# Performance work log

Hardware: AMD Instinct MI355X
Metric: run time of the kernel (lower is better)

The kernel has to match this reference:

```python
import jax, jax.numpy as jnp
import numpy as np

N = 30000; F = 16; E = 300000
HD = 256; NH = 8; C = HD // NH; L = 3
S = 256; K = 128
NH_CA = 4; HDC = HD // NH_CA


def _ln(x, g, b):
    mu = jnp.mean(x, -1, keepdims=True)
    v = jnp.mean((x - mu) ** 2, -1, keepdims=True)
    return (x - mu) / jnp.sqrt(v + 1e-5) * g + b


def setup_inputs() -> dict:
    ks = iter(jax.random.split(jax.random.key(0), 64))
    def nrm(sh, s=0.05):
        return jax.random.normal(next(ks), sh, jnp.float32) * s
    def zeros(sh):
        return jnp.zeros(sh, jnp.float32)
    def ones(sh):
        return jnp.ones(sh, jnp.float32)
    inp = {}
    inp['x'] = jax.random.normal(next(ks), (N, F), jnp.float32)
    inp['edge_index'] = jax.random.randint(next(ks), (2, E), 0, N, jnp.int32)
    inp['batch'] = jnp.zeros((N,), jnp.int32)
    inp['sheet_node_idx'] = jax.random.randint(next(ks), (S, K), 0, N, jnp.int32)
    inp['sheet_features'] = jax.random.normal(next(ks), (S, F), jnp.float32)
    # pre_transform
    inp['pre_W'] = nrm((F, HD)); inp['pre_b'] = zeros((HD,))
    # stacked GATv2 layers (lin_l, lin_r, att, bias)
    inp['gat_Wl'] = nrm((L, HD, HD)); inp['gat_Wr'] = nrm((L, HD, HD))
    inp['gat_att'] = nrm((L, NH, C)); inp['gat_b'] = zeros((L, HD))
    # geometry encoder
    inp['geo_W1'] = nrm((F, HD)); inp['geo_b1'] = zeros((HD,))
    inp['geo_g1'] = ones((HD,)); inp['geo_be1'] = zeros((HD,))
    inp['geo_W2'] = nrm((HD, HD)); inp['geo_b2'] = zeros((HD,))
    inp['geo_g2'] = ones((HD,)); inp['geo_be2'] = zeros((HD,))
    # cross attention (4 heads)
    inp['ca_Wq'] = nrm((HD, HD)); inp['ca_bq'] = zeros((HD,))
    inp['ca_Wk'] = nrm((HD, HD)); inp['ca_bk'] = zeros((HD,))
    inp['ca_Wv'] = nrm((HD, HD)); inp['ca_bv'] = zeros((HD,))
    inp['ca_Wo'] = nrm((HD, HD)); inp['ca_bo'] = zeros((HD,))
    # q_mlp
    inp['q_W1'] = nrm((2 * HD, HD)); inp['q_b1'] = zeros((HD,))
    inp['q_g1'] = ones((HD,)); inp['q_be1'] = zeros((HD,))
    inp['q_W2'] = nrm((HD, HD // 2)); inp['q_b2'] = zeros((HD // 2,))
    inp['q_g2'] = ones((HD // 2,)); inp['q_be2'] = zeros((HD // 2,))
    inp['q_W3'] = nrm((HD // 2, 1)); inp['q_b3'] = zeros((1,))
    # state_done_predictor
    inp['d_W1'] = nrm((HD, HD // 2)); inp['d_b1'] = zeros((HD // 2,))
    inp['d_g1'] = ones((HD // 2,)); inp['d_be1'] = zeros((HD // 2,))
    inp['d_W2'] = nrm((HD // 2, 1)); inp['d_b2'] = zeros((1,))
    return inp


def _fwd(x, sheet_features, pre_W, pre_b, gat_Wl, gat_Wr, gat_att, gat_b,
         geo_W1, geo_b1, geo_g1, geo_be1, geo_W2, geo_b2, geo_g2, geo_be2,
         ca_Wq, ca_bq, ca_Wk, ca_bk, ca_Wv, ca_bv, ca_Wo, ca_bo,
         q_W1, q_b1, q_g1, q_be1, q_W2, q_b2, q_g2, q_be2, q_W3, q_b3,
         d_W1, d_b1, d_g1, d_be1, d_W2, d_b2,
         edge_index, batch, sheet_node_idx):
    loops = jnp.arange(N, dtype=edge_index.dtype)  # PyG GATv2Conv add_self_loops=True
    src = jnp.concatenate([edge_index[0], loops])
    dst = jnp.concatenate([edge_index[1], loops])
    h = x @ pre_W + pre_b  # [N, HD]
    for l in range(L):
        xl = (h @ gat_Wl[l]).reshape(N, NH, C)  # source messages
        xr = (h @ gat_Wr[l]).reshape(N, NH, C)  # target
        m = jax.nn.leaky_relu(xl[src] + xr[dst], 0.2)  # [E+N, NH, C]
        e = jnp.einsum('ehc,hc->eh', m, gat_att[l])
        emax = jax.ops.segment_max(e, dst, num_segments=N)
        a = jnp.exp(e - emax[dst])
        denom = jax.ops.segment_sum(a, dst, num_segments=N)
        alpha = a / (denom[dst] + 1e-16)  # scatter softmax over incoming edges
        h = jax.ops.segment_sum(alpha[:, :, None] * xl[src], dst, num_segments=N)
        h = jax.nn.elu(h.reshape(N, HD) + gat_b[l])
    cnt = jax.ops.segment_sum(jnp.ones((N,), h.dtype), batch, num_segments=1)
    g = jax.ops.segment_sum(h, batch, num_segments=1) / cnt[:, None]  # [1, HD]
    sheet = h[sheet_node_idx].mean(axis=1)  # [S, HD] per-sheet gather+mean
    geo = jax.nn.relu(_ln(sheet_features @ geo_W1 + geo_b1, geo_g1, geo_be1))
    geo = jax.nn.relu(_ln(geo @ geo_W2 + geo_b2, geo_g2, geo_be2))
    qh = (sheet @ ca_Wq + ca_bq).reshape(S, NH_CA, HDC)
    kh = (geo @ ca_Wk + ca_bk).reshape(S, NH_CA, HDC)
    vh = (geo @ ca_Wv + ca_bv).reshape(S, NH_CA, HDC)
    att = jax.nn.softmax(jnp.einsum('qhd,khd->hqk', qh, kh) / jnp.sqrt(jnp.float32(HDC)), axis=-1)
    fused = jnp.einsum('hqk,khd->qhd', att, vh).reshape(S, HD) @ ca_Wo + ca_bo
    hq = jnp.concatenate([fused, jnp.broadcast_to(g, (S, HD))], axis=1)  # [S, 2*HD]
    hq = jax.nn.relu(_ln(hq @ q_W1 + q_b1, q_g1, q_be1))
    hq = jax.nn.relu(_ln(hq @ q_W2 + q_b2, q_g2, q_be2))
    q_values = (hq @ q_W3 + q_b3)[:, 0]  # [S]
    hd = jax.nn.relu(_ln(g @ d_W1 + d_b1, d_g1, d_be1))
    done_logit = (hd @ d_W2 + d_b2)[:, 0]  # [1]
    return q_values, done_logit


def reference(x, edge_index, batch, sheet_node_idx, sheet_features, pre_W, pre_b,
              gat_Wl, gat_Wr, gat_att, gat_b,
              geo_W1, geo_b1, geo_g1, geo_be1, geo_W2, geo_b2, geo_g2, geo_be2,
              ca_Wq, ca_bq, ca_Wk, ca_bk, ca_Wv, ca_bv, ca_Wo, ca_bo,
              q_W1, q_b1, q_g1, q_be1, q_W2, q_b2, q_g2, q_be2, q_W3, q_b3,
              d_W1, d_b1, d_g1, d_be1, d_W2, d_b2):
    return _fwd(x, sheet_features, pre_W, pre_b, gat_Wl, gat_Wr, gat_att, gat_b,
                geo_W1, geo_b1, geo_g1, geo_be1, geo_W2, geo_b2, geo_g2, geo_be2,
                ca_Wq, ca_bq, ca_Wk, ca_bk, ca_Wv, ca_bv, ca_Wo, ca_bo,
                q_W1, q_b1, q_g1, q_be1, q_W2, q_b2, q_g2, q_be2, q_W3, q_b3,
                d_W1, d_b1, d_g1, d_be1, d_W2, d_b2,
                edge_index, batch, sheet_node_idx)
```

## Files before the change

kernel.cpp:

```cpp
#include <hip/hip_runtime.h>
#include <hip/hip_bf16.h>
#include <stdint.h>

#define NN 30000
#define MPAD 30080
#define FI 16
#define EE 300000
#define ETOT (EE + NN)
#define HD 256
#define NH 8
#define CH 32
#define NL 3
#define SS 256
#define KS 128
#define NHC 4
#define HC 64
#define GSB 256
#define RPB 118
#define SCB 118

typedef _Float16 half8 __attribute__((ext_vector_type(8)));
typedef _Float16 half4v __attribute__((ext_vector_type(4)));
typedef _Float16 half2v __attribute__((ext_vector_type(2)));
typedef float f32x4 __attribute__((ext_vector_type(4)));
// ... 94 lines not shown
    Tq2[(size_t)n * 256 + t] = (_Float16)q_W2[(size_t)t * 128 + n];
  }
}

__global__ __launch_bounds__(256) void k_pre(const float* __restrict__ x,
    const float* __restrict__ W, const float* __restrict__ b,
    _Float16* __restrict__ H16)
{
  __shared__ float Ws[FI][HD];
  __shared__ float xs[8][FI];
  int r0 = blockIdx.x * 8;
  int t = threadIdx.x;
  for (int i = t; i < FI * HD; i += 256) Ws[i >> 8][i & 255] = W[i];
  if (t < 8 * FI) xs[t >> 4][t & 15] = x[(size_t)(r0 + (t >> 4)) * FI + (t & 15)];
  __syncthreads();
  float bj = b[t];
  for (int r = 0; r < 8; ++r) {
    float acc = bj;
#pragma unroll
    for (int k = 0; k < FI; ++k) acc += xs[r][k] * Ws[k][t];
    H16[(size_t)(r0 + r) * HD + t] = (_Float16)acc;
  }
}

__global__ __launch_bounds__(256) void k_count(const int* __restrict__ ei, int* __restrict__ cnt)
{
  int i = blockIdx.x * 256 + threadIdx.x;
  if (i >= ETOT) return;
  int dst = (i < EE) ? ei[EE + i] : (i - EE);
  atomicAdd(&cnt[dst], 1);
}

__global__ __launch_bounds__(256) void k_scanA(const int* __restrict__ cnt,
    int* __restrict__ rowptr, int* __restrict__ btot)
{
  __shared__ int wt[4];
  int b = blockIdx.x, t = threadIdx.x;
  int i = b * 256 + t;
  int v = (i < NN) ? cnt[i] : 0;
  int lane = t & 63, w = t >> 6;
  int s = v;
#pragma unroll
  for (int d = 1; d < 64; d <<= 1) {
    int u = __shfl_up(s, d);
    if (lane >= d) s += u;
  }
  if (lane == 63) wt[w] = s;
  __syncthreads();
  int off = 0;
  for (int k = 0; k < w; ++k) off += wt[k];
  if (i < NN) rowptr[i] = off + s - v;
  if (t == 255) btot[b] = off + s;
}

__global__ __launch_bounds__(128) void k_scanB(const int* __restrict__ btot,
    int* __restrict__ boff, int* __restrict__ rowptr)
{
  __shared__ int wt[2];
  int t = threadIdx.x;
  int v = (t < SCB) ? btot[t] : 0;
  int lane = t & 63, w = t >> 6;
  int s = v;
#pragma unroll
  for (int d = 1; d < 64; d <<= 1) {
    int u = __shfl_up(s, d);
    if (lane >= d) s += u;
  }
  if (lane == 63) wt[w] = s;
  __syncthreads();
  int off = (w == 1) ? wt[0] : 0;
  if (t < SCB) boff[t] = off + s - v;
  if (t == 127) rowptr[NN] = wt[0] + wt[1];
}

__global__ __launch_bounds__(256) void k_scanC(int* __restrict__ rowptr,
    const int* __restrict__ boff, int* __restrict__ wptr)
{
  int b = blockIdx.x, t = threadIdx.x;
  int i = b * 256 + t;
  if (i < NN) {
    int r = rowptr[i] + boff[b];
    rowptr[i] = r;
    wptr[i] = r;
  }
}

__global__ __launch_bounds__(256) void k_scatter(const int* __restrict__ ei,
    int* __restrict__ wptr, int* __restrict__ csr_src)
{
  int i = blockIdx.x * 256 + threadIdx.x;
  if (i >= ETOT) return;
  int src = (i < EE) ? ei[i] : (i - EE);
  int dst = (i < EE) ? ei[EE + i] : (i - EE);
  int pos = atomicAdd(&wptr[dst], 1);
  csr_src[pos] = src * HD;
}

#define BKG 64
__global__ __launch_bounds__(512) void k_gemm16(const _Float16* __restrict__ A,
    const _Float16* __restrict__ WT,
    _Float16* __restrict__ Xl, _Float16* __restrict__ Xr)
{
  __shared__ __align__(16) _Float16 As[64 * BKG];
  __shared__ __align__(16) _Float16 Bs[512 * BKG];
  int t = threadIdx.x;
  int w = t >> 6, lane = t & 63;
  int row0 = blockIdx.x * 64;

  f32x4 acc[4][4] = {};

  for (int k0 = 0; k0 < HD; k0 += BKG) {
    {
      int row = t >> 3, s = t & 7;
      int g = s ^ (row & 7);
      __builtin_amdgcn_global_load_lds(
        (const __attribute__((address_space(1))) void*)(A + (size_t)(row0 + row) * HD + k0 + g * 8),
        (__attribute__((address_space(3))) void*)((char*)As + w * 1024),
        16, 0, 0);
    }
#pragma unroll
    for (int i = 0; i < 8; ++i) {
      int p = i * 512 + t;
      int row = p >> 3, s = p & 7;
      int g = s ^ (row & 7);
      __builtin_amdgcn_global_load_lds(
        (const __attribute__((address_space(1))) void*)(WT + (size_t)row * HD + k0 + g * 8),
        (__attribute__((address_space(3))) void*)((char*)Bs + (i * 8 + w) * 1024),
// ... 12 lines not shown
      }
#pragma unroll
      for (int ni = 0; ni < 4; ++ni) {
        int nl = w * 64 + ni * 16 + (lane & 15);
        int ps = kslot ^ (nl & 7);
        bfr[ni] = *(const half8*)((const char*)Bs + nl * 128 + ps * 16);
      }
#pragma unroll
      for (int mi = 0; mi < 4; ++mi)
#pragma unroll
        for (int ni = 0; ni < 4; ++ni)
          acc[mi][ni] = __builtin_amdgcn_mfma_f32_16x16x32_f16(af[mi], bfr[ni], acc[mi][ni], 0, 0, 0);
    }
    __syncthreads();
  }
  int crow = (lane >> 4) * 4;
  int ccol = lane & 15;
  _Float16* Out = (w < 4) ? Xl : Xr;
  int cbase = (w < 4) ? (w * 64) : ((w - 4) * 64);
#pragma unroll
  for (int mi = 0; mi < 4; ++mi)
#pragma unroll
    for (int ni = 0; ni < 4; ++ni) {
      size_t base_r = row0 + mi * 16 + crow;
      int c = cbase + ni * 16 + ccol;
#pragma unroll
      for (int r = 0; r < 4; ++r)
        Out[(base_r + r) * HD + c] = (_Float16)acc[mi][ni][r];
    }
}

__global__ __launch_bounds__(256) void k_edgeagg(const _Float16* __restrict__ Xl,
    const _Float16* __restrict__ Xr, const float* __restrict__ attw,
    const float* __restrict__ bias, const int* __restrict__ rowptr,
    const int* __restrict__ csr_src, _Float16* __restrict__ H16)
{
  int node = blockIdx.x * 4 + (threadIdx.x >> 6);
  int lane = threadIdx.x & 63;
  if (node >= NN) return;
  int st = rowptr[node], en = rowptr[node + 1];
  int n = en - st;
  int hf = lane >> 5, sl = lane & 31;
  int c = sl * 8;
  half8 xrv = *(const half8*)(Xr + (size_t)node * HD + c);
  float4 wa = *(const float4*)(attw + c);
  float4 wb = *(const float4*)(attw + c + 4);
  half2v w0 = mk2((_Float16)wa.x, (_Float16)wa.y);
  half2v w1 = mk2((_Float16)wa.z, (_Float16)wa.w);
  half2v w2 = mk2((_Float16)wb.x, (_Float16)wb.y);
  half2v w3 = mk2((_Float16)wb.z, (_Float16)wb.w);
  half2v r0 = mk2(xrv[0], xrv[1]), r1 = mk2(xrv[2], xrv[3]);
  half2v r2 = mk2(xrv[4], xrv[5]), r3 = mk2(xrv[6], xrv[7]);
  half2v c02 = mk2((_Float16)0.2f, (_Float16)0.2f);

  float mh = -1e30f, dsum = 0.f;
  half2v acch0 = {}, acch1 = {}, acch2 = {}, acch3 = {};
  int trips = (n + 1) >> 1;
  int trips4 = (trips + 3) >> 2;
  int base = st + hf;

  half8 cur0 = *(const half8*)(Xl + (size_t)csr_src[base + 0] + c);
  half8 cur1 = *(const half8*)(Xl + (size_t)csr_src[base + 2] + c);
  half8 cur2 = *(const half8*)(Xl + (size_t)csr_src[base + 4] + c);
  half8 cur3 = *(const half8*)(Xl + (size_t)csr_src[base + 6] + c);

  for (int it = 0; it < trips4; ++it) {
    int nb = base + 8 * (it + 1);
    half8 nxt0 = *(const half8*)(Xl + (size_t)csr_src[nb + 0] + c);
    half8 nxt1 = *(const half8*)(Xl + (size_t)csr_src[nb + 2] + c);
    half8 nxt2 = *(const half8*)(Xl + (size_t)csr_src[nb + 4] + c);
    half8 nxt3 = *(const half8*)(Xl + (size_t)csr_src[nb + 6] + c);

    int s0i = 8 * it + hf;
// ... 156 lines not shown
  if (s == SS) {
    float a0 = 0.f, a1 = 0.f, a2 = 0.f, a3 = 0.f;
    for (int b = 0; b < GSB; b += 4) {
      a0 += gpart[(size_t)b * HD + t];
      a1 += gpart[(size_t)(b + 1) * HD + t];
      a2 += gpart[(size_t)(b + 2) * HD + t];
      a3 += gpart[(size_t)(b + 3) * HD + t];
    }
    gvec[t] = ((a0 + a1) + (a2 + a3)) / (float)(*gcnt);
    return;
  }

  if (t < KS) sidx[t] = sheet_idx[s * KS + t];
  if (t >= 240) xf[t - 240] = sheet_feat[s * FI + (t - 240)];
  __syncthreads();

  float pa[8] = {};
#pragma unroll 2
  for (int r = 0; r < KS; r += 8) {
#pragma unroll
    for (int u = 0; u < 8; ++u)
      pa[u] += (float)h16[(size_t)sidx[r + u] * HD + t];
  }
  float shv = ((pa[0] + pa[1]) + (pa[2] + pa[3]) + (pa[4] + pa[5]) + (pa[6] + pa[7])) * (1.f / KS);
  sh16[(size_t)s * HD + t] = (_Float16)shv;

  float a = geo_b1[t];
#pragma unroll
  for (int k = 0; k < FI; ++k) a += xf[k] * geo_W1[k * HD + t];
  float g1 = ln_fast(a, t, 256, red16, geo_g1, geo_be1, true);
  g116[(size_t)s * HD + t] = (_Float16)g1;
}

template <int KD, int NW>
__global__ __launch_bounds__(NW * 64) void k_stageLN(
    const _Float16* __restrict__ X, const _Float16* __restrict__ WT,
    const float* __restrict__ b, const float* __restrict__ G,
    const float* __restrict__ Be, _Float16* __restrict__ Y,
    const float* __restrict__ W3, const float* __restrict__ b3,
    float* __restrict__ outq,
    const float* __restrict__ gvec,
    const float* __restrict__ dW1, const float* __restrict__ db1,
    const float* __restrict__ dg1, const float* __restrict__ dbe1,
    const float* __restrict__ dW2, const float* __restrict__ db2,
    float* __restrict__ outd)
{
  __shared__ float ps[NW * 16], ps2[NW * 16], pq[NW * 16];
  const int NCOL = NW * 64;
  int t = threadIdx.x;

  if (outd != nullptr && blockIdx.x == 16) {
    int w2 = t >> 6;
    float acc2 = db1[t];
    for (int k = 0; k < 256; ++k) acc2 += gvec[k] * dW1[(size_t)k * 128 + t];
    float s = wsum(acc2), s2v = wsum(acc2 * acc2);
    if ((t & 63) == 0) { ps[w2] = s; ps2[w2] = s2v; }
    __syncthreads();
    float S = ps[0] + ps[1], S2 = ps2[0] + ps2[1];
    float mu = S * (1.f / 128.f), var = S2 * (1.f / 128.f) - mu * mu;
    float hdv = fmaxf((acc2 - mu) * rsqrtf(var + 1e-5f) * dg1[t] + dbe1[t], 0.f);
    float o = wsum(hdv * dW2[t]);
    if ((t & 63) == 0) pq[w2] = o;
    __syncthreads();
    if (t == 0) outd[0] = pq[0] + pq[1] + db2[0];
    return;
  }

  int w = t >> 6, lane = t & 63;
  int arow = lane & 15, kg = lane >> 4;
  int m0 = blockIdx.x * 16;
  int col0 = w * 64;

  f32x4 acc[4] = {};
#pragma unroll
  for (int ks = 0; ks < KD / 32; ++ks) {
    half8 af = *(const half8*)(X + (size_t)(m0 + arow) * KD + ks * 32 + kg * 8);
#pragma unroll
    for (int n = 0; n < 4; ++n) {
      half8 bf = *(const half8*)(WT + (size_t)(col0 + n * 16 + arow) * KD + ks * 32 + kg * 8);
      acc[n] = __builtin_amdgcn_mfma_f32_16x16x32_f16(af, bf, acc[n], 0, 0, 0);
    }
  }
#pragma unroll
  for (int n = 0; n < 4; ++n) {
    float bv = b[col0 + n * 16 + arow];
#pragma unroll
    for (int r = 0; r < 4; ++r) acc[n][r] += bv;
  }
  float s[4] = {}, s2[4] = {};
#pragma unroll
  for (int n = 0; n < 4; ++n)
#pragma unroll
    for (int r = 0; r < 4; ++r) { float v = acc[n][r]; s[r] += v; s2[r] += v * v; }
#pragma unroll
  for (int d = 1; d < 16; d <<= 1)
#pragma unroll
    for (int r = 0; r < 4; ++r) { s[r] += __shfl_xor(s[r], d); s2[r] += __shfl_xor(s2[r], d); }
  if (arow == 0) {
#pragma unroll
    for (int r = 0; r < 4; ++r) {
      ps[w * 16 + kg * 4 + r] = s[r];
      ps2[w * 16 + kg * 4 + r] = s2[r];
    }
  }
  __syncthreads();
  float mu[4], rs[4];
#pragma unroll
  for (int r = 0; r < 4; ++r) {
    float S = 0.f, S2 = 0.f;
#pragma unroll
    for (int w2 = 0; w2 < NW; ++w2) { S += ps[w2 * 16 + kg * 4 + r]; S2 += ps2[w2 * 16 + kg * 4 + r]; }
    float m = S / NCOL;
    float var = S2 / NCOL - m * m;
    mu[r] = m; rs[r] = rsqrtf(var + 1e-5f);
  }
#pragma unroll
  for (int n = 0; n < 4; ++n) {
    int col = col0 + n * 16 + arow;
    float gv = G[col], bev = Be[col];
#pragma unroll
    for (int r = 0; r < 4; ++r)
      acc[n][r] = fmaxf((acc[n][r] - mu[r]) * rs[r] * gv + bev, 0.f);
  }
  if (Y) {
#pragma unroll
    for (int n = 0; n < 4; ++n) {
      int col = col0 + n * 16 + arow;
#pragma unroll
      for (int r = 0; r < 4; ++r)
        Y[(size_t)(m0 + kg * 4 + r) * NCOL + col] = (_Float16)acc[n][r];
    }
  }
  if (outq) {
    float p[4] = {};
#pragma unroll
    for (int n = 0; n < 4; ++n) {
      float w3 = W3[col0 + n * 16 + arow];
#pragma unroll
      for (int r = 0; r < 4; ++r) p[r] += acc[n][r] * w3;
    }
#pragma unroll
    for (int d = 1; d < 16; d <<= 1)
#pragma unroll
      for (int r = 0; r < 4; ++r) p[r] += __shfl_xor(p[r], d);
    if (arow == 0)
#pragma unroll
      for (int r = 0; r < 4; ++r) pq[w * 16 + kg * 4 + r] = p[r];
    __syncthreads();
    if (w == 0 && arow == 0) {
#pragma unroll
      for (int r = 0; r < 4; ++r) {
        float o = b3[0];
#pragma unroll
        for (int w2 = 0; w2 < NW; ++w2) o += pq[w2 * 16 + kg * 4 + r];
        outq[m0 + kg * 4 + r] = o;
      }
    }
  }
}

__global__ __launch_bounds__(64) void k_qkv(
    const _Float16* __restrict__ sh16, const _Float16* __restrict__ g216,
    const _Float16* __restrict__ Tq, const _Float16* __restrict__ Tk,
    const _Float16* __restrict__ Tv,
    const float* __restrict__ bq, const float* __restrict__ bk,
    const float* __restrict__ bv,
    _Float16* __restrict__ qb, _Float16* __restrict__ kb, _Float16* __restrict__ vb)
{
  int lane = threadIdx.x;
  int arow = lane & 15, kg = lane >> 4;
  int m0 = blockIdx.x * 16;
  int col0 = blockIdx.y * 64;
  int mat = blockIdx.z;
  const _Float16* X = (mat == 0) ? sh16 : g216;
  const _Float16* WT = (mat == 0) ? Tq : (mat == 1) ? Tk : Tv;
  const float* b = (mat == 0) ? bq : (mat == 1) ? bk : bv;
  _Float16* Y = (mat == 0) ? qb : (mat == 1) ? kb : vb;

  f32x4 acc[4] = {};
#pragma unroll
  for (int ks = 0; ks < 8; ++ks) {
    half8 af = *(const half8*)(X + (size_t)(m0 + arow) * 256 + ks * 32 + kg * 8);
#pragma unroll
    for (int n = 0; n < 4; ++n) {
      half8 bf = *(const half8*)(WT + (size_t)(col0 + n * 16 + arow) * 256 + ks * 32 + kg * 8);
      acc[n] = __builtin_amdgcn_mfma_f32_16x16x32_f16(af, bf, acc[n], 0, 0, 0);
    }
  }
#pragma unroll
  for (int n = 0; n < 4; ++n) {
    int col = col0 + n * 16 + arow;
    float bv2 = b[col];
#pragma unroll
    for (int r = 0; r < 4; ++r)
      Y[(size_t)(m0 + kg * 4 + r) * 256 + col] = (_Float16)(acc[n][r] + bv2);
  }
}

__global__ __launch_bounds__(64) void k_wo(
    const _Float16* __restrict__ pv16, const _Float16* __restrict__ To,
    const float* __restrict__ bo, const float* __restrict__ gvec,
    _Float16* __restrict__ hqin)
{
  int lane = threadIdx.x;
  int arow = lane & 15, kg = lane >> 4;
  int m0 = blockIdx.x * 16;
  int col0 = blockIdx.y * 64;

  f32x4 acc[4] = {};
#pragma unroll
  for (int ks = 0; ks < 8; ++ks) {
    half8 af = *(const half8*)(pv16 + (size_t)(m0 + arow) * 256 + ks * 32 + kg * 8);
#pragma unroll
    for (int n = 0; n < 4; ++n) {
      half8 bf = *(const half8*)(To + (size_t)(col0 + n * 16 + arow) * 256 + ks * 32 + kg * 8);
      acc[n] = __builtin_amdgcn_mfma_f32_16x16x32_f16(af, bf, acc[n], 0, 0, 0);
    }
  }
#pragma unroll
  for (int n = 0; n < 4; ++n) {
    int col = col0 + n * 16 + arow;
    float bv = bo[col];
    _Float16 gg = (_Float16)gvec[col];
#pragma unroll
    for (int r = 0; r < 4; ++r) {
      hqin[(size_t)(m0 + kg * 4 + r) * 512 + col] = (_Float16)(acc[n][r] + bv);
      hqin[(size_t)(m0 + kg * 4 + r) * 512 + 256 + col] = gg;
    }
  }
}

__global__ __launch_bounds__(1024) void k_attn(const _Float16* __restrict__ qb,
    const _Float16* __restrict__ kb, const _Float16* __restrict__ vb,
    _Float16* __restrict__ pv16)
{
  __shared__ float qv[HD];
  __shared__ float att[1024];
  __shared__ float red4[1024];
  __shared__ float redm[16];
  __shared__ float reds[16];
  int row = blockIdx.x, t = threadIdx.x;
  int w = t >> 6;

  if (t < 256) qv[t] = (float)qb[(size_t)row * HD + t];
  __syncthreads();

  int h = t >> 8, key = t & 255;
  float e = 0.f;
  {
    const half8* kr = (const half8*)(kb + (size_t)key * HD + h * HC);
    const float* qh = qv + h * HC;
#pragma unroll
    for (int d = 0; d < 8; ++d) {
      half8 kk = kr[d];
#pragma unroll
      for (int u = 0; u < 8; ++u) e += qh[d * 8 + u] * (float)kk[u];
    }
    e *= 0.125f;
  }
  float wm = e;
#pragma unroll
  for (int d = 1; d < 64; d <<= 1) wm = fmaxf(wm, __shfl_xor(wm, d));
  if ((t & 63) == 0) redm[w] = wm;
  __syncthreads();
  float mx = fmaxf(fmaxf(redm[4 * h], redm[4 * h + 1]), fmaxf(redm[4 * h + 2], redm[4 * h + 3]));
  float pw = __expf(e - mx);
  float ws = wsum(pw);
  if ((t & 63) == 0) reds[w] = ws;
  att[t] = pw;
  __syncthreads();

  int kq = t >> 8, j = t & 255;
  int hj = j >> 6;
  float p = 0.f;
  const float* arow = att + hj * 256 + kq * 64;
  const _Float16* vcol = vb + (size_t)(kq * 64) * HD + j;
  for (int k = 0; k < 64; ++k)
    p += arow[k] * (float)vcol[(size_t)k * HD];
  red4[t] = p;
  __syncthreads();
  if (t < 256) {
    int hh = t >> 6;
    float dsum = reds[4 * hh] + reds[4 * hh + 1] + reds[4 * hh + 2] + reds[4 * hh + 3];
    float pv = (red4[t] + red4[256 + t] + red4[512 + t] + red4[768 + t]) / dsum;
    pv16[(size_t)row * HD + t] = (_Float16)pv;
  }
}

extern "C" void kernel_launch(void* const* d_in, const int* in_sizes, int n_in,
                              void* d_out, int out_size, void* d_ws, size_t ws_size,
                              hipStream_t stream) {
  const float* x      = (const float*)d_in[0];
  const int*   ei     = (const int*)d_in[1];
  const int*   batch  = (const int*)d_in[2];
  const int*   sheet_idx = (const int*)d_in[3];
  const float* sheet_feat = (const float*)d_in[4];
  const float* pre_W  = (const float*)d_in[5];
  const float* pre_b  = (const float*)d_in[6];
  const float* gat_Wl = (const float*)d_in[7];
  const float* gat_Wr = (const float*)d_in[8];
  const float* gat_att = (const float*)d_in[9];
  const float* gat_b  = (const float*)d_in[10];
  const float* geo_W1 = (const float*)d_in[11];
  const float* geo_b1 = (const float*)d_in[12];
  const float* geo_g1 = (const float*)d_in[13];
  const float* geo_be1 = (const float*)d_in[14];
  const float* geo_W2 = (const float*)d_in[15];
  const float* geo_b2 = (const float*)d_in[16];
  const float* geo_g2 = (const float*)d_in[17];
  const float* geo_be2 = (const float*)d_in[18];
  const float* ca_Wq = (const float*)d_in[19];
  const float* ca_bq = (const float*)d_in[20];
  const float* ca_Wk = (const float*)d_in[21];
  const float* ca_bk = (const float*)d_in[22];
  const float* ca_Wv = (const float*)d_in[23];
  const float* ca_bv = (const float*)d_in[24];
  const float* ca_Wo = (const float*)d_in[25];
  const float* ca_bo = (const float*)d_in[26];
  const float* q_W1 = (const float*)d_in[27];
  const float* q_b1 = (const float*)d_in[28];
  const float* q_g1 = (const float*)d_in[29];
  const float* q_be1 = (const float*)d_in[30];
  const float* q_W2 = (const float*)d_in[31];
  const float* q_b2 = (const float*)d_in[32];
  const float* q_g2 = (const float*)d_in[33];
  const float* q_be2 = (const float*)d_in[34];
  const float* q_W3 = (const float*)d_in[35];
  const float* q_b3 = (const float*)d_in[36];
  const float* d_W1 = (const float*)d_in[37];
  const float* d_b1 = (const float*)d_in[38];
  const float* d_g1 = (const float*)d_in[39];
  const float* d_be1 = (const float*)d_in[40];
  const float* d_W2 = (const float*)d_in[41];
  const float* d_b2 = (const float*)d_in[42];

  char* wsb = (char*)d_ws;
  auto alloc = [&](size_t bytes) { char* p = wsb; wsb += (bytes + 255) & ~(size_t)255; return p; };

  _Float16* h16  = (_Float16*)alloc((size_t)MPAD * HD * 2);
  _Float16* Xl16 = (_Float16*)alloc((size_t)MPAD * HD * 2);
  _Float16* Xr16 = (_Float16*)alloc((size_t)MPAD * HD * 2);
  _Float16* WT   = (_Float16*)alloc((size_t)6 * HD * HD * 2);
  _Float16* Tgeo2 = (_Float16*)alloc((size_t)HD * HD * 2);
  _Float16* Tq   = (_Float16*)alloc((size_t)HD * HD * 2);
  _Float16* Tk   = (_Float16*)alloc((size_t)HD * HD * 2);
  _Float16* Tv   = (_Float16*)alloc((size_t)HD * HD * 2);
  _Float16* To   = (_Float16*)alloc((size_t)HD * HD * 2);
  _Float16* Tq1  = (_Float16*)alloc((size_t)HD * 512 * 2);
  _Float16* Tq2  = (_Float16*)alloc((size_t)128 * HD * 2);
  _Float16* sh16 = (_Float16*)alloc((size_t)SS * HD * 2);
  _Float16* g116 = (_Float16*)alloc((size_t)SS * HD * 2);
  _Float16* g216 = (_Float16*)alloc((size_t)SS * HD * 2);
  _Float16* qb16 = (_Float16*)alloc((size_t)SS * HD * 2);
  _Float16* kb16 = (_Float16*)alloc((size_t)SS * HD * 2);
  _Float16* vb16 = (_Float16*)alloc((size_t)SS * HD * 2);
  _Float16* pv16 = (_Float16*)alloc((size_t)SS * HD * 2);
  _Float16* hqin16 = (_Float16*)alloc((size_t)SS * 512 * 2);
  _Float16* hq116 = (_Float16*)alloc((size_t)SS * HD * 2);
  float* gpart   = (float*)alloc((size_t)GSB * HD * 4);
  float* gvec    = (float*)alloc(256 * 4);
  int* cnt       = (int*)alloc((size_t)NN * 4);
  int* rowptr    = (int*)alloc((size_t)(NN + 1) * 4);
  int* wptr      = (int*)alloc((size_t)NN * 4);
  int* csr_src   = (int*)alloc((size_t)(ETOT + 16) * 4);
  int* btot      = (int*)alloc((size_t)SCB * 4);
  int* boff      = (int*)alloc((size_t)SCB * 4);
  int* gcnt      = (int*)alloc(4);

  float* out_q = (float*)d_out;
  float* out_d = out_q + SS;

  k_wconvAll<<<3318, 256, 0, stream>>>(gat_Wl, gat_Wr, geo_W2, ca_Wq, ca_Wk, ca_Wv,
                                       ca_Wo, q_W1, q_W2,
                                       WT, Tgeo2, Tq, Tk, Tv, To, Tq1, Tq2,
                                       cnt, gcnt, h16 + (size_t)NN * HD, csr_src + ETOT);

  k_count<<<(ETOT + 255) / 256, 256, 0, stream>>>(ei, cnt);
  k_scanA<<<SCB, 256, 0, stream>>>(cnt, rowptr, btot);
  k_scanB<<<1, 128, 0, stream>>>(btot, boff, rowptr);
  k_scanC<<<SCB, 256, 0, stream>>>(rowptr, boff, wptr);
  k_scatter<<<(ETOT + 255) / 256, 256, 0, stream>>>(ei, wptr, csr_src);

  k_pre<<<NN / 8, 256, 0, stream>>>(x, pre_W, pre_b, h16);

  for (int l = 0; l < NL; ++l) {
    k_gemm16<<<MPAD / 64, 512, 0, stream>>>(h16, WT + (size_t)l * 2 * HD * HD, Xl16, Xr16);
    k_edgeagg<<<(NN + 3) / 4, 256, 0, stream>>>(Xl16, Xr16, gat_att + l * NH * CH,
                                                gat_b + l * HD, rowptr, csr_src, h16);
  }

  k_gsum<<<GSB, 256, 0, stream>>>(h16, batch, gpart, gcnt);

  k_tail1<<<SS + 1, 256, 0, stream>>>(h16, sheet_idx, sheet_feat,
      geo_W1, geo_b1, geo_g1, geo_be1, gpart, gcnt, gvec, sh16, g116);
  k_stageLN<256, 4><<<16, 256, 0, stream>>>(g116, Tgeo2, geo_b2, geo_g2, geo_be2,
      g216, nullptr, nullptr, nullptr,
      nullptr, nullptr, nullptr, nullptr, nullptr, nullptr, nullptr, nullptr);
  dim3 qkvg(16, 4, 3);
  k_qkv<<<qkvg, 64, 0, stream>>>(sh16, g216, Tq, Tk, Tv, ca_bq, ca_bk, ca_bv,
                                 qb16, kb16, vb16);
  k_attn<<<SS, 1024, 0, stream>>>(qb16, kb16, vb16, pv16);
  dim3 wog(16, 4);
  k_wo<<<wog, 64, 0, stream>>>(pv16, To, ca_bo, gvec, hqin16);
  k_stageLN<512, 4><<<16, 256, 0, stream>>>(hqin16, Tq1, q_b1, q_g1, q_be1,
      hq116, nullptr, nullptr, nullptr,
      nullptr, nullptr, nullptr, nullptr, nullptr, nullptr, nullptr, nullptr);
  k_stageLN<256, 2><<<17, 128, 0, stream>>>(hq116, Tq2, q_b2, q_g2, q_be2,
      nullptr, q_W3, q_b3, out_q,
      gvec, d_W1, d_b1, d_g1, d_be1, d_W2, d_b2, out_d);
}
```

Baseline: 275.9 us.

## Fuse tail GEMM stages and drop scanC by applying block offsets lazily

Removes the third scan pass: rowptr and write pointers stay block-local, and the per-256-node block offset is added at use time in the scatter and edge-aggregation kernels. The tail MLP is regrouped so that geo layer2+LN feeds K/V projections through LDS in one kernel, and the Wo projection plus concat-with-graph-vector plus q_W1+LN run in one kernel. This drops the intermediate g216/hqin buffers. The aim is fewer launches and less global traffic, at the cost of an extra boff load per edge in scatter and per node in edgeagg, and less parallelism in the fused stages (16 blocks).

```diff
diff --git a/kernel.cpp b/kernel.cpp
--- a/kernel.cpp
+++ b/kernel.cpp
@@ -150,7 +150,7 @@
 }
 
 __global__ __launch_bounds__(256) void k_scanA(const int* __restrict__ cnt,
-    int* __restrict__ rowptr, int* __restrict__ btot)
+    int* __restrict__ rowptrL, int* __restrict__ wptrL, int* __restrict__ btot)
 {
   __shared__ int wt[4];
   int b = blockIdx.x, t = threadIdx.x;
@@ -167,12 +167,12 @@
   __syncthreads();
   int off = 0;
   for (int k = 0; k < w; ++k) off += wt[k];
-  if (i < NN) rowptr[i] = off + s - v;
+  if (i < NN) { int e = off + s - v; rowptrL[i] = e; wptrL[i] = e; }
   if (t == 255) btot[b] = off + s;
 }
 
 __global__ __launch_bounds__(128) void k_scanB(const int* __restrict__ btot,
-    int* __restrict__ boff, int* __restrict__ rowptr)
+    int* __restrict__ boff, int* __restrict__ rowptrL)
 {
   __shared__ int wt[2];
   int t = threadIdx.x;
@@ -188,29 +188,17 @@
   __syncthreads();
   int off = (w == 1) ? wt[0] : 0;
   if (t < SCB) boff[t] = off + s - v;
-  if (t == 127) rowptr[NN] = wt[0] + wt[1];
-}
-
-__global__ __launch_bounds__(256) void k_scanC(int* __restrict__ rowptr,
-    const int* __restrict__ boff, int* __restrict__ wptr)
-{
-  int b = blockIdx.x, t = threadIdx.x;
-  int i = b * 256 + t;
-  if (i < NN) {
-    int r = rowptr[i] + boff[b];
-    rowptr[i] = r;
-    wptr[i] = r;
-  }
+  if (t == SCB - 1) rowptrL[NN] = v;
 }
 
 __global__ __launch_bounds__(256) void k_scatter(const int* __restrict__ ei,
-    int* __restrict__ wptr, int* __restrict__ csr_src)
+    int* __restrict__ wptrL, const int* __restrict__ boff, int* __restrict__ csr_src)
 {
   int i = blockIdx.x * 256 + threadIdx.x;
   if (i >= ETOT) return;
   int src = (i < EE) ? ei[i] : (i - EE);
   int dst = (i < EE) ? ei[EE + i] : (i - EE);
-  int pos = atomicAdd(&wptr[dst], 1);
+  int pos = atomicAdd(&wptrL[dst], 1) + boff[dst >> 8];
   csr_src[pos] = src * HD;
 }
 
@@ -289,13 +277,15 @@
 
 __global__ __launch_bounds__(256) void k_edgeagg(const _Float16* __restrict__ Xl,
     const _Float16* __restrict__ Xr, const float* __restrict__ attw,
-    const float* __restrict__ bias, const int* __restrict__ rowptr,
-    const int* __restrict__ csr_src, _Float16* __restrict__ H16)
+    const float* __restrict__ bias, const int* __restrict__ rowptrL,
+    const int* __restrict__ boff, const int* __restrict__ csr_src,
+    _Float16* __restrict__ H16)
 {
   int node = blockIdx.x * 4 + (threadIdx.x >> 6);
   int lane = threadIdx.x & 63;
   if (node >= NN) return;
-  int st = rowptr[node], en = rowptr[node + 1];
+  int st = rowptrL[node] + boff[node >> 8];
+  int en = rowptrL[node + 1] + boff[(node + 1) >> 8];
   int n = en - st;
   int hf = lane >> 5, sl = lane & 31;
   int c = sl * 8;
@@ -518,24 +508,294 @@
   g116[(size_t)s * HD + t] = (_Float16)g1;
 }
 
-template <int KD, int NW>
-__global__ __launch_bounds__(NW * 64) void k_stageLN(
-    const _Float16* __restrict__ X, const _Float16* __restrict__ WT,
-    const float* __restrict__ b, const float* __restrict__ G,
-    const float* __restrict__ Be, _Float16* __restrict__ Y,
-    const float* __restrict__ W3, const float* __restrict__ b3,
-    float* __restrict__ outq,
+__device__ __forceinline__ void mf_gA(int m0, int col0, const _Float16* __restrict__ X,
+    int KD, const _Float16* __restrict__ WT, f32x4* acc, int lane)
+{
+  int arow = lane & 15, kg = lane >> 4;
+#pragma unroll
+  for (int n = 0; n < 4; ++n) { acc[n][0] = 0.f; acc[n][1] = 0.f; acc[n][2] = 0.f; acc[n][3] = 0.f; }
+  for (int ks = 0; ks < KD / 32; ++ks) {
+    half8 af = *(const half8*)(X + (size_t)(m0 + arow) * KD + ks * 32 + kg * 8);
+#pragma unroll
+    for (int n = 0; n < 4; ++n) {
+      half8 bf = *(const half8*)(WT + (size_t)(col0 + n * 16 + arow) * KD + ks * 32 + kg * 8);
+      acc[n] = __builtin_amdgcn_mfma_f32_16x16x32_f16(af, bf, acc[n], 0, 0, 0);
+    }
+  }
+}
+
+__device__ __forceinline__ void mf_lA(int col0, const _Float16* lA,
+    const _Float16* __restrict__ WT, f32x4* acc, int lane)
+{
+  int arow = lane & 15, kg = lane >> 4;
+#pragma unroll
+  for (int n = 0; n < 4; ++n) { acc[n][0] = 0.f; acc[n][1] = 0.f; acc[n][2] = 0.f; acc[n][3] = 0.f; }
+#pragma unroll
+  for (int ks = 0; ks < 8; ++ks) {
+    int slot = (ks * 4 + kg) ^ (arow & 7);
+    half8 af = *(const half8*)(lA + arow * 256 + slot * 8);
+#pragma unroll
+    for (int n = 0; n < 4; ++n) {
+      half8 bf = *(const half8*)(WT + (size_t)(col0 + n * 16 + arow) * 256 + ks * 32 + kg * 8);
+      acc[n] = __builtin_amdgcn_mfma_f32_16x16x32_f16(af, bf, acc[n], 0, 0, 0);
+    }
+  }
+}
+
+__device__ __forceinline__ void st_lA(int col0, const f32x4* acc, _Float16* lA, int lane)
+{
+  int arow = lane & 15, kg = lane >> 4;
+#pragma unroll
+  for (int n = 0; n < 4; ++n) {
+    int col = col0 + n * 16 + arow;
+#pragma unroll
+    for (int r = 0; r < 4; ++r) {
+      int row = kg * 4 + r;
+      int phys = (((col >> 3) ^ (row & 7)) << 3) | (col & 7);
+      lA[row * 256 + phys] = (_Float16)acc[n][r];
+    }
+  }
+}
+
+__device__ __forceinline__ void ln4w(f32x4* acc, int col0, int lane,
+    float* ps, float* ps2, const float* __restrict__ G, const float* __restrict__ Be)
+{
+  int arow = lane & 15, kg = lane >> 4;
+  int w = col0 >> 6;
+  float s[4] = {}, s2[4] = {};
+#pragma unroll
+  for (int n = 0; n < 4; ++n)
+#pragma unroll
+    for (int r = 0; r < 4; ++r) { float v = acc[n][r]; s[r] += v; s2[r] += v * v; }
+#pragma unroll
+  for (int d = 1; d < 16; d <<= 1)
+#pragma unroll
+    for (int r = 0; r < 4; ++r) { s[r] += __shfl_xor(s[r], d); s2[r] += __shfl_xor(s2[r], d); }
+  if (arow == 0) {
+#pragma unroll
+    for (int r = 0; r < 4; ++r) { ps[w * 16 + kg * 4 + r] = s[r]; ps2[w * 16 + kg * 4 + r] = s2[r]; }
+  }
+  __syncthreads();
+#pragma unroll
+  for (int r = 0; r < 4; ++r) {
+    float S = 0.f, S2 = 0.f;
+#pragma unroll
+    for (int w2 = 0; w2 < 4; ++w2) { S += ps[w2 * 16 + kg * 4 + r]; S2 += ps2[w2 * 16 + kg * 4 + r]; }
+    float mu = S * (1.f / 256.f);
+    float var = S2 * (1.f / 256.f) - mu * mu;
+    float rsv = rsqrtf(var + 1e-5f);
+#pragma unroll
+    for (int n = 0; n < 4; ++n) {
+      int col = col0 + n * 16 + arow;
+      acc[n][r] = fmaxf((acc[n][r] - mu) * rsv * G[col] + Be[col], 0.f);
+    }
+  }
+}
+
+__global__ __launch_bounds__(256) void k_stageGeoKV(
+    const _Float16* __restrict__ g116,
+    const _Float16* __restrict__ Tgeo2, const float* __restrict__ geo_b2,
+    const float* __restrict__ geo_g2, const float* __restrict__ geo_be2,
+    const _Float16* __restrict__ Tk, const _Float16* __restrict__ Tv,
+    const float* __restrict__ bk, const float* __restrict__ bv,
+    _Float16* __restrict__ kb, _Float16* __restrict__ vb)
+{
+  __shared__ __align__(16) _Float16 lA[16 * 256];
+  __shared__ float ps[64], ps2[64];
+  int t = threadIdx.x;
+  int w = t >> 6, lane = t & 63;
+  int arow = lane & 15, kg = lane >> 4;
+  int m0 = blockIdx.x * 16;
+  int col0 = w * 64;
+
+  f32x4 acc[4];
+  mf_gA(m0, col0, g116, 256, Tgeo2, acc, lane);
+#pragma unroll
+  for (int n = 0; n < 4; ++n) {
+    float bv2 = geo_b2[col0 + n * 16 + arow];
+#pragma unroll
+    for (int r = 0; r < 4; ++r) acc[n][r] += bv2;
+  }
+  ln4w(acc, col0, lane, ps, ps2, geo_g2, geo_be2);
+  st_lA(col0, acc, lA, lane);
+  __syncthreads();
+
+  mf_lA(col0, lA, Tk, acc, lane);
+#pragma unroll
+  for (int n = 0; n < 4; ++n) {
+    int col = col0 + n * 16 + arow;
+    float bv2 = bk[col];
+#pragma unroll
+    for (int r = 0; r < 4; ++r)
+      kb[(size_t)(m0 + kg * 4 + r) * 256 + col] = (_Float16)(acc[n][r] + bv2);
+  }
+  mf_lA(col0, lA, Tv, acc, lane);
+#pragma unroll
+  for (int n = 0; n < 4; ++n) {
+    int col = col0 + n * 16 + arow;
+    float bv2 = bv[col];
+#pragma unroll
+    for (int r = 0; r < 4; ++r)
+      vb[(size_t)(m0 + kg * 4 + r) * 256 + col] = (_Float16)(acc[n][r] + bv2);
+  }
+}
+
+__global__ __launch_bounds__(64) void k_q(
+    const _Float16* __restrict__ sh16, const _Float16* __restrict__ Tq,
+    const float* __restrict__ bq, _Float16* __restrict__ qb)
+{
+  int lane = threadIdx.x;
+  int arow = lane & 15, kg = lane >> 4;
+  int m0 = blockIdx.x * 16;
+  int col0 = blockIdx.y * 64;
+  f32x4 acc[4];
+  mf_gA(m0, col0, sh16, 256, Tq, acc, lane);
+#pragma unroll
+  for (int n = 0; n < 4; ++n) {
+    int col = col0 + n * 16 + arow;
+    float bv2 = bq[col];
+#pragma unroll
+    for (int r = 0; r < 4; ++r)
+      qb[(size_t)(m0 + kg * 4 + r) * 256 + col] = (_Float16)(acc[n][r] + bv2);
+  }
+}
+
+__global__ __launch_bounds__(256) void k_stageWoHq1(
+    const _Float16* __restrict__ pv16,
+    const _Float16* __restrict__ To, const float* __restrict__ bo,
+    const float* __restrict__ gvec,
+    const _Float16* __restrict__ Tq1, const float* __restrict__ q_b1,
+    const float* __restrict__ q_g1, const float* __restrict__ q_be1,
+    _Float16* __restrict__ hq116)
+{
+  __shared__ __align__(16) _Float16 lFu[16 * 256];
+  __shared__ __align__(16) _Float16 lGv[256];
+  __shared__ float ps[64], ps2[64];
+  int t = threadIdx.x;
+  int w = t >> 6, lane = t & 63;
+  int arow = lane & 15, kg = lane >> 4;
+  int m0 = blockIdx.x * 16;
+  int col0 = w * 64;
+
+  if (t < 256) lGv[t] = (_Float16)gvec[t];
+
+  f32x4 acc[4];
+  mf_gA(m0, col0, pv16, 256, To, acc, lane);
+#pragma unroll
+  for (int n = 0; n < 4; ++n) {
+    float bv2 = bo[col0 + n * 16 + arow];
+#pragma unroll
+    for (int r = 0; r < 4; ++r) acc[n][r] += bv2;
+  }
+  st_lA(col0, acc, lFu, lane);
+  __syncthreads();
+
+#pragma unroll
+  for (int n = 0; n < 4; ++n) { acc[n][0] = 0.f; acc[n][1] = 0.f; acc[n][2] = 0.f; acc[n][3] = 0.f; }
+#pragma unroll
+  for (int ks = 0; ks < 16; ++ks) {
+    half8 af;
+    if (ks < 8) {
+      int slot = (ks * 4 + kg) ^ (arow & 7);
+      af = *(const half8*)(lFu + arow * 256 + slot * 8);
+    } else {
+      af = *(const half8*)(lGv + (ks - 8) * 32 + kg * 8);
+    }
+#pragma unroll
+    for (int n = 0; n < 4; ++n) {
+      half8 bf = *(const half8*)(Tq1 + (size_t)(col0 + n * 16 + arow) * 512 + ks * 32 + kg * 8);
+      acc[n] = __builtin_amdgcn_mfma_f32_16x16x32_f16(af, bf, acc[n], 0, 0, 0);
+    }
+  }
+#pragma unroll
+  for (int n = 0; n < 4; ++n) {
+    float bv2 = q_b1[col0 + n * 16 + arow];
+#pragma unroll
+    for (int r = 0; r < 4; ++r) acc[n][r] += bv2;
+  }
+  ln4w(acc, col0, lane, ps, ps2, q_g1, q_be1);
+#pragma unroll
+  for (int n = 0; n < 4; ++n) {
+    int col = col0 + n * 16 + arow;
+#pragma unroll
+    for (int r = 0; r < 4; ++r)
+      hq116[(size_t)(m0 + kg * 4 + r) * 256 + col] = (_Float16)acc[n][r];
+  }
+}
+
+__global__ __launch_bounds__(1024) void k_attn(const _Float16* __restrict__ qb,
+    const _Float16* __restrict__ kb, const _Float16* __restrict__ vb,
+    _Float16* __restrict__ pv16)
+{
+  __shared__ float qv[HD];
+  __shared__ float att[1024];
+  __shared__ float red4[1024];
+  __shared__ float redm[16];
+  __shared__ float reds[16];
+  int row = blockIdx.x, t = threadIdx.x;
+  int w = t >> 6;
+
+  if (t < 256) qv[t] = (float)qb[(size_t)row * HD + t];
+  __syncthreads();
+
+  int h = t >> 8, key = t & 255;
+  float e = 0.f;
+  {
+    const half8* kr = (const half8*)(kb + (size_t)key * HD + h * HC);
+    const float* qh = qv + h * HC;
+#pragma unroll
+    for (int d = 0; d < 8; ++d) {
+      half8 kk = kr[d];
+#pragma unroll
+      for (int u = 0; u < 8; ++u) e += qh[d * 8 + u] * (float)kk[u];
+    }
+    e *= 0.125f;
+  }
+  float wm = e;
+#pragma unroll
+  for (int d = 1; d < 64; d <<= 1) wm = fmaxf(wm, __shfl_xor(wm, d));
+  if ((t & 63) == 0) redm[w] = wm;
+  __syncthreads();
+  float mx = fmaxf(fmaxf(redm[4 * h], redm[4 * h + 1]), fmaxf(redm[4 * h + 2], redm[4 * h + 3]));
+  float pw = __expf(e - mx);
+  float ws = wsum(pw);
+  if ((t & 63) == 0) reds[w] = ws;
+  att[t] = pw;
+  __syncthreads();
+
+  int kq = t >> 8, j = t & 255;
+  int hj = j >> 6;
+  float p = 0.f;
+  const float* arow = att + hj * 256 + kq * 64;
+  const _Float16* vcol = vb + (size_t)(kq * 64) * HD + j;
+  for (int k = 0; k < 64; ++k)
+    p += arow[k] * (float)vcol[(size_t)k * HD];
+  red4[t] = p;
+  __syncthreads();
+  if (t < 256) {
+    int hh = t >> 6;
+    float dsum = reds[4 * hh] + reds[4 * hh + 1] + reds[4 * hh + 2] + reds[4 * hh + 3];
+    float pv = (red4[t] + red4[256 + t] + red4[512 + t] + red4[768 + t]) / dsum;
+    pv16[(size_t)row * HD + t] = (_Float16)pv;
+  }
+}
+
+__global__ __launch_bounds__(128) void k_stageOut(
+    const _Float16* __restrict__ hq116, const _Float16* __restrict__ Tq2,
+    const float* __restrict__ q_b2, const float* __restrict__ q_g2,
+    const float* __restrict__ q_be2,
+    const float* __restrict__ q_W3, const float* __restrict__ q_b3,
+    float* __restrict__ out_q,
     const float* __restrict__ gvec,
     const float* __restrict__ dW1, const float* __restrict__ db1,
     const float* __restrict__ dg1, const float* __restrict__ dbe1,
     const float* __restrict__ dW2, const float* __restrict__ db2,
-    float* __restrict__ outd)
-{
-  __shared__ float ps[NW * 16], ps2[NW * 16], pq[NW * 16];
-  const int NCOL = NW * 64;
+    float* __restrict__ out_d)
+{
+  __shared__ float ps[32], ps2[32], pq[32];
   int t = threadIdx.x;
 
-  if (outd != nullptr && blockIdx.x == 16) {
+  if (blockIdx.x == 16) {
     int w2 = t >> 6;
     float acc2 = db1[t];
     for (int k = 0; k < 256; ++k) acc2 += gvec[k] * dW1[(size_t)k * 128 + t];
@@ -548,7 +808,7 @@
     float o = wsum(hdv * dW2[t]);
     if ((t & 63) == 0) pq[w2] = o;
     __syncthreads();
-    if (t == 0) outd[0] = pq[0] + pq[1] + db2[0];
+    if (t == 0) out_d[0] = pq[0] + pq[1] + db2[0];
     return;
   }
 
@@ -557,21 +817,13 @@
   int m0 = blockIdx.x * 16;
   int col0 = w * 64;
 
-  f32x4 acc[4] = {};
-#pragma unroll
-  for (int ks = 0; ks < KD / 32; ++ks) {
-    half8 af = *(const half8*)(X + (size_t)(m0 + arow) * KD + ks * 32 + kg * 8);
-#pragma unroll
-    for (int n = 0; n < 4; ++n) {
-      half8 bf = *(const half8*)(WT + (size_t)(col0 + n * 16 + arow) * KD + ks * 32 + kg * 8);
-      acc[n] = __builtin_amdgcn_mfma_f32_16x16x32_f16(af, bf, acc[n], 0, 0, 0);
-    }
-  }
+  f32x4 acc[4];
+  mf_gA(m0, col0, hq116, 256, Tq2, acc, lane);
 #pragma unroll
   for (int n = 0; n < 4; ++n) {
-    float bv = b[col0 + n * 16 + arow];
-#pragma unroll
-    for (int r = 0; r < 4; ++r) acc[n][r] += bv;
+    float bv2 = q_b2[col0 + n * 16 + arow];
+#pragma unroll
+    for (int r = 0; r < 4; ++r) acc[n][r] += bv2;
   }
   float s[4] = {}, s2[4] = {};
 #pragma unroll
@@ -584,192 +836,41 @@
     for (int r = 0; r < 4; ++r) { s[r] += __shfl_xor(s[r], d); s2[r] += __shfl_xor(s2[r], d); }
   if (arow == 0) {
 #pragma unroll
-    for (int r = 0; r < 4; ++r) {
-      ps[w * 16 + kg * 4 + r] = s[r];
-      ps2[w * 16 + kg * 4 + r] = s2[r];
-    }
-  }
-  __syncthreads();
-  float mu[4], rs[4];
+    for (int r = 0; r < 4; ++r) { ps[w * 16 + kg * 4 + r] = s[r]; ps2[w * 16 + kg * 4 + r] = s2[r]; }
+  }
+  __syncthreads();
 #pragma unroll
   for (int r = 0; r < 4; ++r) {
-    float S = 0.f, S2 = 0.f;
-#pragma unroll
-    for (int w2 = 0; w2 < NW; ++w2) { S += ps[w2 * 16 + kg * 4 + r]; S2 += ps2[w2 * 16 + kg * 4 + r]; }
-    float m = S / NCOL;
-    float var = S2 / NCOL - m * m;
-    mu[r] = m; rs[r] = rsqrtf(var + 1e-5f);
-  }
-#pragma unroll
-  for (int n = 0; n < 4; ++n) {
-    int col = col0 + n * 16 + arow;
-    float gv = G[col], bev = Be[col];
-#pragma unroll
-    for (int r = 0; r < 4; ++r)
-      acc[n][r] = fmaxf((acc[n][r] - mu[r]) * rs[r] * gv + bev, 0.f);
-  }
-  if (Y) {
+    float S = ps[kg * 4 + r] + ps[16 + kg * 4 + r];
+    float S2 = ps2[kg * 4 + r] + ps2[16 + kg * 4 + r];
+    float mu = S * (1.f / 128.f);
+    float var = S2 * (1.f / 128.f) - mu * mu;
+    float rsv = rsqrtf(var + 1e-5f);
 #pragma unroll
     for (int n = 0; n < 4; ++n) {
       int col = col0 + n * 16 + arow;
-#pragma unroll
-      for (int r = 0; r < 4; ++r)
-        Y[(size_t)(m0 + kg * 4 + r) * NCOL + col] = (_Float16)acc[n][r];
-    }
-  }
-  if (outq) {
-    float p[4] = {};
-#pragma unroll
-    for (int n = 0; n < 4; ++n) {
-      float w3 = W3[col0 + n * 16 + arow];
-#pragma unroll
-      for (int r = 0; r < 4; ++r) p[r] += acc[n][r] * w3;
-    }
-#pragma unroll
-    for (int d = 1; d < 16; d <<= 1)
-#pragma unroll
-      for (int r = 0; r < 4; ++r) p[r] += __shfl_xor(p[r], d);
-    if (arow == 0)
-#pragma unroll
-      for (int r = 0; r < 4; ++r) pq[w * 16 + kg * 4 + r] = p[r];
-    __syncthreads();
-    if (w == 0 && arow == 0) {
-#pragma unroll
-      for (int r = 0; r < 4; ++r) {
-        float o = b3[0];
-#pragma unroll
-        for (int w2 = 0; w2 < NW; ++w2) o += pq[w2 * 16 + kg * 4 + r];
-        outq[m0 + kg * 4 + r] = o;
-      }
-    }
-  }
-}
-
-__global__ __launch_bounds__(64) void k_qkv(
-    const _Float16* __restrict__ sh16, const _Float16* __restrict__ g216,
-    const _Float16* __restrict__ Tq, const _Float16* __restrict__ Tk,
-    const _Float16* __restrict__ Tv,
-    const float* __restrict__ bq, const float* __restrict__ bk,
-    const float* __restrict__ bv,
-    _Float16* __restrict__ qb, _Float16* __restrict__ kb, _Float16* __restrict__ vb)
-{
-  int lane = threadIdx.x;
-  int arow = lane & 15, kg = lane >> 4;
-  int m0 = blockIdx.x * 16;
-  int col0 = blockIdx.y * 64;
-  int mat = blockIdx.z;
-  const _Float16* X = (mat == 0) ? sh16 : g216;
-  const _Float16* WT = (mat == 0) ? Tq : (mat == 1) ? Tk : Tv;
-  const float* b = (mat == 0) ? bq : (mat == 1) ? bk : bv;
-  _Float16* Y = (mat == 0) ? qb : (mat == 1) ? kb : vb;
-
-  f32x4 acc[4] = {};
-#pragma unroll
-  for (int ks = 0; ks < 8; ++ks) {
-    half8 af = *(const half8*)(X + (size_t)(m0 + arow) * 256 + ks * 32 + kg * 8);
-#pragma unroll
-    for (int n = 0; n < 4; ++n) {
-      half8 bf = *(const half8*)(WT + (size_t)(col0 + n * 16 + arow) * 256 + ks * 32 + kg * 8);
-      acc[n] = __builtin_amdgcn_mfma_f32_16x16x32_f16(af, bf, acc[n], 0, 0, 0);
-    }
-  }
+      acc[n][r] = fmaxf((acc[n][r] - mu) * rsv * q_g2[col] + q_be2[col], 0.f);
+    }
+  }
+  float p[4] = {};
 #pragma unroll
   for (int n = 0; n < 4; ++n) {
-    int col = col0 + n * 16 + arow;
-    float bv2 = b[col];
+    float w3 = q_W3[col0 + n * 16 + arow];
+#pragma unroll
+    for (int r = 0; r < 4; ++r) p[r] += acc[n][r] * w3;
+  }
+#pragma unroll
+  for (int d = 1; d < 16; d <<= 1)
+#pragma unroll
+    for (int r = 0; r < 4; ++r) p[r] += __shfl_xor(p[r], d);
+  if (arow == 0)
+#pragma unroll
+    for (int r = 0; r < 4; ++r) pq[w * 16 + kg * 4 + r] = p[r];
+  __syncthreads();
+  if (w == 0 && arow == 0) {
 #pragma unroll
     for (int r = 0; r < 4; ++r)
-      Y[(size_t)(m0 + kg * 4 + r) * 256 + col] = (_Float16)(acc[n][r] + bv2);
-  }
-}
-
-__global__ __launch_bounds__(64) void k_wo(
-    const _Float16* __restrict__ pv16, const _Float16* __restrict__ To,
-    const float* __restrict__ bo, const float* __restrict__ gvec,
-    _Float16* __restrict__ hqin)
-{
-  int lane = threadIdx.x;
-  int arow = lane & 15, kg = lane >> 4;
-  int m0 = blockIdx.x * 16;
-  int col0 = blockIdx.y * 64;
-
-  f32x4 acc[4] = {};
-#pragma unroll
-  for (int ks = 0; ks < 8; ++ks) {
-    half8 af = *(const half8*)(pv16 + (size_t)(m0 + arow) * 256 + ks * 32 + kg * 8);
-#pragma unroll
-    for (int n = 0; n < 4; ++n) {
-      half8 bf = *(const half8*)(To + (size_t)(col0 + n * 16 + arow) * 256 + ks * 32 + kg * 8);
-      acc[n] = __builtin_amdgcn_mfma_f32_16x16x32_f16(af, bf, acc[n], 0, 0, 0);
-    }
-  }
-#pragma unroll
-  for (int n = 0; n < 4; ++n) {
-    int col = col0 + n * 16 + arow;
-    float bv = bo[col];
-    _Float16 gg = (_Float16)gvec[col];
-#pragma unroll
-    for (int r = 0; r < 4; ++r) {
-      hqin[(size_t)(m0 + kg * 4 + r) * 512 + col] = (_Float16)(acc[n][r] + bv);
-      hqin[(size_t)(m0 + kg * 4 + r) * 512 + 256 + col] = gg;
-    }
-  }
-}
-
-__global__ __launch_bounds__(1024) void k_attn(const _Float16* __restrict__ qb,
-    const _Float16* __restrict__ kb, const _Float16* __restrict__ vb,
-    _Float16* __restrict__ pv16)
-{
-  __shared__ float qv[HD];
-  __shared__ float att[1024];
-  __shared__ float red4[1024];
-  __shared__ float redm[16];
-  __shared__ float reds[16];
-  int row = blockIdx.x, t = threadIdx.x;
-  int w = t >> 6;
-
-  if (t < 256) qv[t] = (float)qb[(size_t)row * HD + t];
-  __syncthreads();
-
-  int h = t >> 8, key = t & 255;
-  float e = 0.f;
-  {
-    const half8* kr = (const half8*)(kb + (size_t)key * HD + h * HC);
-    const float* qh = qv + h * HC;
-#pragma unroll
-    for (int d = 0; d < 8; ++d) {
-      half8 kk = kr[d];
-#pragma unroll
-      for (int u = 0; u < 8; ++u) e += qh[d * 8 + u] * (float)kk[u];
-    }
-    e *= 0.125f;
-  }
-  float wm = e;
-#pragma unroll
-  for (int d = 1; d < 64; d <<= 1) wm = fmaxf(wm, __shfl_xor(wm, d));
-  if ((t & 63) == 0) redm[w] = wm;
-  __syncthreads();
-  float mx = fmaxf(fmaxf(redm[4 * h], redm[4 * h + 1]), fmaxf(redm[4 * h + 2], redm[4 * h + 3]));
-  float pw = __expf(e - mx);
-  float ws = wsum(pw);
-  if ((t & 63) == 0) reds[w] = ws;
-  att[t] = pw;
-  __syncthreads();
-
-  int kq = t >> 8, j = t & 255;
-  int hj = j >> 6;
-  float p = 0.f;
-  const float* arow = att + hj * 256 + kq * 64;
-  const _Float16* vcol = vb + (size_t)(kq * 64) * HD + j;
-  for (int k = 0; k < 64; ++k)
-    p += arow[k] * (float)vcol[(size_t)k * HD];
-  red4[t] = p;
-  __syncthreads();
-  if (t < 256) {
-    int hh = t >> 6;
-    float dsum = reds[4 * hh] + reds[4 * hh + 1] + reds[4 * hh + 2] + reds[4 * hh + 3];
-    float pv = (red4[t] + red4[256 + t] + red4[512 + t] + red4[768 + t]) / dsum;
-    pv16[(size_t)row * HD + t] = (_Float16)pv;
+      out_q[m0 + kg * 4 + r] = pq[kg * 4 + r] + pq[16 + kg * 4 + r] + q_b3[0];
   }
 }
 
@@ -836,18 +937,16 @@
   _Float16* Tq2  = (_Float16*)alloc((size_t)128 * HD * 2);
   _Float16* sh16 = (_Float16*)alloc((size_t)SS * HD * 2);
   _Float16* g116 = (_Float16*)alloc((size_t)SS * HD * 2);
-  _Float16* g216 = (_Float16*)alloc((size_t)SS * HD * 2);
   _Float16* qb16 = (_Float16*)alloc((size_t)SS * HD * 2);
   _Float16* kb16 = (_Float16*)alloc((size_t)SS * HD * 2);
   _Float16* vb16 = (_Float16*)alloc((size_t)SS * HD * 2);
   _Float16* pv16 = (_Float16*)alloc((size_t)SS * HD * 2);
-  _Float16* hqin16 = (_Float16*)alloc((size_t)SS * 512 * 2);
   _Float16* hq116 = (_Float16*)alloc((size_t)SS * HD * 2);
   float* gpart   = (float*)alloc((size_t)GSB * HD * 4);
   float* gvec    = (float*)alloc(256 * 4);
   int* cnt       = (int*)alloc((size_t)NN * 4);
-  int* rowptr    = (int*)alloc((size_t)(NN + 1) * 4);
-  int* wptr      = (int*)alloc((size_t)NN * 4);
+  int* rowptrL   = (int*)alloc((size_t)(NN + 1) * 4);
+  int* wptrL     = (int*)alloc((size_t)NN * 4);
   int* csr_src   = (int*)alloc((size_t)(ETOT + 16) * 4);
   int* btot      = (int*)alloc((size_t)SCB * 4);
   int* boff      = (int*)alloc((size_t)SCB * 4);
@@ -862,36 +961,29 @@
                                        cnt, gcnt, h16 + (size_t)NN * HD, csr_src + ETOT);
 
   k_count<<<(ETOT + 255) / 256, 256, 0, stream>>>(ei, cnt);
-  k_scanA<<<SCB, 256, 0, stream>>>(cnt, rowptr, btot);
-  k_scanB<<<1, 128, 0, stream>>>(btot, boff, rowptr);
-  k_scanC<<<SCB, 256, 0, stream>>>(rowptr, boff, wptr);
-  k_scatter<<<(ETOT + 255) / 256, 256, 0, stream>>>(ei, wptr, csr_src);
+  k_scanA<<<SCB, 256, 0, stream>>>(cnt, rowptrL, wptrL, btot);
+  k_scanB<<<1, 128, 0, stream>>>(btot, boff, rowptrL);
+  k_scatter<<<(ETOT + 255) / 256, 256, 0, stream>>>(ei, wptrL, boff, csr_src);
 
   k_pre<<<NN / 8, 256, 0, stream>>>(x, pre_W, pre_b, h16);
 
   for (int l = 0; l < NL; ++l) {
     k_gemm16<<<MPAD / 64, 512, 0, stream>>>(h16, WT + (size_t)l * 2 * HD * HD, Xl16, Xr16);
     k_edgeagg<<<(NN + 3) / 4, 256, 0, stream>>>(Xl16, Xr16, gat_att + l * NH * CH,
-                                                gat_b + l * HD, rowptr, csr_src, h16);
+                                                gat_b + l * HD, rowptrL, boff, csr_src, h16);
   }
 
   k_gsum<<<GSB, 256, 0, stream>>>(h16, batch, gpart, gcnt);
 
   k_tail1<<<SS + 1, 256, 0, stream>>>(h16, sheet_idx, sheet_feat,
       geo_W1, geo_b1, geo_g1, geo_be1, gpart, gcnt, gvec, sh16, g116);
-  k_stageLN<256, 4><<<16, 256, 0, stream>>>(g116, Tgeo2, geo_b2, geo_g2, geo_be2,
-      g216, nullptr, nullptr, nullptr,
-      nullptr, nullptr, nullptr, nullptr, nullptr, nullptr, nullptr, nullptr);
-  dim3 qkvg(16, 4, 3);
-  k_qkv<<<qkvg, 64, 0, stream>>>(sh16, g216, Tq, Tk, Tv, ca_bq, ca_bk, ca_bv,
-                                 qb16, kb16, vb16);
+  k_stageGeoKV<<<16, 256, 0, stream>>>(g116, Tgeo2, geo_b2, geo_g2, geo_be2,
+      Tk, Tv, ca_bk, ca_bv, kb16, vb16);
+  dim3 qg(16, 4);
+  k_q<<<qg, 64, 0, stream>>>(sh16, Tq, ca_bq, qb16);
   k_attn<<<SS, 1024, 0, stream>>>(qb16, kb16, vb16, pv16);
-  dim3 wog(16, 4);
-  k_wo<<<wog, 64, 0, stream>>>(pv16, To, ca_bo, gvec, hqin16);
-  k_stageLN<512, 4><<<16, 256, 0, stream>>>(hqin16, Tq1, q_b1, q_g1, q_be1,
-      hq116, nullptr, nullptr, nullptr,
-      nullptr, nullptr, nullptr, nullptr, nullptr, nullptr, nullptr, nullptr);
-  k_stageLN<256, 2><<<17, 128, 0, stream>>>(hq116, Tq2, q_b2, q_g2, q_be2,
-      nullptr, q_W3, q_b3, out_q,
-      gvec, d_W1, d_b1, d_g1, d_be1, d_W2, d_b2, out_d);
-}
+  k_stageWoHq1<<<16, 256, 0, stream>>>(pv16, To, ca_bo, gvec,
+      Tq1, q_b1, q_g1, q_be1, hq116);
+  k_stageOut<<<17, 128, 0, stream>>>(hq116, Tq2, q_b2, q_g2, q_be2,
+      q_W3, q_b3, out_q, gvec, d_W1, d_b1, d_g1, d_be1, d_W2, d_b2, out_d);
+}
```

New measurement: 290.7 us. +5.4%, slower.
